# Kernel tuning notes

Hardware: AMD Instinct MI355X
Metric: run time of the kernel (lower is better)

Reference implementation:

```python
import jax, jax.numpy as jnp
import numpy as np

D_MODEL = 1024
N_HEADS = 16
HEAD_DIM = D_MODEL // N_HEADS
EPS = 1e-5


def _rope_tables(T, dim, dtype):
    inv_freq = 1.0 / (10000.0 ** (np.arange(0, dim, 2, dtype=np.float32) / dim))
    t = np.arange(T, dtype=np.float32)
    freqs = np.einsum('i,j->ij', t, inv_freq)            # [T, dim/2]
    emb = np.concatenate([freqs, freqs], axis=-1)        # [T, dim]
    return jnp.asarray(np.cos(emb), dtype), jnp.asarray(np.sin(emb), dtype)


def _rotate(x, cos, sin):
    # x: [B, T, H, hd]; cos/sin: [T, hd] broadcast over B, H
    c = cos[None, :, None, :]
    s = sin[None, :, None, :]
    x1, x2 = jnp.split(x, 2, axis=-1)
    return x * c + jnp.concatenate([-x2, x1], axis=-1) * s


def setup_inputs() -> dict:
    key = jax.random.key(0)
    k1, k2, k3 = jax.random.split(key, 3)
    B, T = 2, 2048
    x = jax.random.normal(k1, (B, T, D_MODEL), jnp.float32)
    norm_w = jnp.ones((D_MODEL,), jnp.float32)
    w_qkv = jax.random.normal(k2, (D_MODEL, 3 * D_MODEL), jnp.float32) * (D_MODEL ** -0.5)
    w_out = jax.random.normal(k3, (D_MODEL, D_MODEL), jnp.float32) * (D_MODEL ** -0.5)
    return {"x": x, "norm_w": norm_w, "w_qkv": w_qkv, "w_out": w_out}


def reference(x, norm_w, w_qkv, w_out):
    B, T, D = x.shape
    residual = x
    # RMSNorm
    h = x * jax.lax.rsqrt(jnp.mean(x * x, axis=-1, keepdims=True) + EPS) * norm_w
    # QKV projection
    qkv = (h @ w_qkv).reshape(B, T, 3, N_HEADS, HEAD_DIM)
    q, k, v = qkv[:, :, 0], qkv[:, :, 1], qkv[:, :, 2]   # [B, T, H, hd]
    # RoPE
    cos, sin = _rope_tables(T, HEAD_DIM, x.dtype)
    q = _rotate(q, cos, sin)
    k = _rotate(k, cos, sin)
    # Non-causal scaled dot-product attention
    scale = HEAD_DIM ** -0.5
    scores = jnp.einsum('bqhd,bkhd->bhqk', q, k) * scale
    attn = jax.nn.softmax(scores, axis=-1)
    out = jnp.einsum('bhqk,bkhd->bqhd', attn, v).reshape(B, T, D)
    return residual + out @ w_out
```

## Files before the change

### kernel.cpp

```cpp
#include <hip/hip_runtime.h>
#include <hip/hip_bf16.h>

typedef float f32x4 __attribute__((ext_vector_type(4)));
typedef __bf16 bf16x8 __attribute__((ext_vector_type(8)));
typedef __bf16 bf16x4 __attribute__((ext_vector_type(4)));

#define D_MODEL 1024
#define T_SEQ   2048
#define NH      16
#define HD      64

__device__ __forceinline__ void gload16(const void* g, void* l) {
    __builtin_amdgcn_global_load_lds(
        (const __attribute__((address_space(1))) unsigned int*)g,
        (__attribute__((address_space(3))) unsigned int*)l, 16, 0, 0);
}

__global__ __launch_bounds__(256) void k_rope_table(float2* __restrict__ tab) {
    int idx = blockIdx.x * 256 + threadIdx.x;
    int t = idx >> 5, i = idx & 31;
    float inv = __builtin_amdgcn_exp2f(-(float)i * 0.41524101186f);
    float ang = (float)t * inv;
    tab[idx] = make_float2(cosf(ang), sinf(ang));
}

__global__ __launch_bounds__(256) void k_rmsnorm(const float* __restrict__ x,
                                                 const float* __restrict__ w,
                                                 __bf16* __restrict__ h) {
    int row = blockIdx.x;
    int tid = threadIdx.x;
    const float4 v = ((const float4*)(x + (size_t)row * D_MODEL))[tid];
    float ss = v.x * v.x + v.y * v.y + v.z * v.z + v.w * v.w;
#pragma unroll
    for (int off = 32; off > 0; off >>= 1) ss += __shfl_down(ss, off, 64);
    __shared__ float red[4];
    if ((tid & 63) == 0) red[tid >> 6] = ss;
    __syncthreads();
    float total = red[0] + red[1] + red[2] + red[3];
    float rms = rsqrtf(total * (1.f / 1024.f) + 1e-5f);
    const float4 wv = ((const float4*)w)[tid];
    bf16x4 o;
    o[0] = (__bf16)(v.x * rms * wv.x);
    o[1] = (__bf16)(v.y * rms * wv.y);
    o[2] = (__bf16)(v.z * rms * wv.z);
    o[3] = (__bf16)(v.w * rms * wv.w);
    ((bf16x4*)(h + (size_t)row * D_MODEL))[tid] = o;
}

__global__ __launch_bounds__(256) void k_transpose_cast(const float* __restrict__ src,
                                                        __bf16* __restrict__ dst,
                                                        int R, int C) {
    __shared__ float tile[32][33];
    int tx = threadIdx.x & 31, ty = threadIdx.x >> 5;
    int c0 = blockIdx.x * 32, r0 = blockIdx.y * 32;
#pragma unroll
    for (int dy = 0; dy < 32; dy += 8)
        tile[ty + dy][tx] = src[(size_t)(r0 + ty + dy) * C + c0 + tx];
    __syncthreads();
#pragma unroll
    for (int dy = 0; dy < 32; dy += 8)
        dst[(size_t)(c0 + ty + dy) * R + r0 + tx] = (__bf16)tile[tx][ty + dy];
}

template <int EPI>
__global__ __launch_bounds__(256) void k_gemm(const __bf16* __restrict__ A,
                                              const __bf16* __restrict__ Bt, int K,
                                              const float2* __restrict__ tab,
                                              __bf16* __restrict__ Qr,
                                              __bf16* __restrict__ Kr,
                                              __bf16* __restrict__ Vt,
                                              const float* __restrict__ resid,
                                              float* __restrict__ outf) {
    __shared__ __bf16 ldsA[128 * 64];
    __shared__ __bf16 ldsB[128 * 64];
    const int tid  = threadIdx.x;
    const int lane = tid & 63;
    const int wave = tid >> 6;
    const int tile_m = blockIdx.y * 128;
    const int tile_n = blockIdx.x * 128;
    const int wm = (wave >> 1) * 64;
    const int wn = (wave & 1) * 64;
    f32x4 acc[4][4] = {};

    const int srow8 = lane >> 3;
    const int sslot = lane & 7;

    for (int k0 = 0; k0 < K; k0 += 64) {
#pragma unroll
        for (int i = 0; i < 4; i++) {
            int rbase = i * 32 + wave * 8;
            int row = rbase + srow8;
            int scol = (sslot ^ (row & 7)) * 8;
            gload16(A  + (size_t)(tile_m + row) * K + k0 + scol,
                    (char*)ldsA + rbase * 128);
            gload16(Bt + (size_t)(tile_n + row) * K + k0 + scol,
                    (char*)ldsB + rbase * 128);
        }
        __syncthreads();
#pragma unroll
        for (int kc = 0; kc < 2; kc++) {
            bf16x8 af[4], bfr[4];
            int s = kc * 4 + (lane >> 4);
#pragma unroll
            for (int mi = 0; mi < 4; mi++) {
                int row = wm + mi * 16 + (lane & 15);
                af[mi] = *(const bf16x8*)((char*)ldsA + row * 128 + ((s ^ (row & 7)) << 4));
            }
#pragma unroll
            for (int nf = 0; nf < 4; nf++) {
                int row = wn + nf * 16 + (lane & 15);
                bfr[nf] = *(const bf16x8*)((char*)ldsB + row * 128 + ((s ^ (row & 7)) << 4));
            }
#pragma unroll
            for (int mi = 0; mi < 4; mi++)
#pragma unroll
                for (int nf = 0; nf < 4; nf++)
                    acc[mi][nf] = __builtin_amdgcn_mfma_f32_16x16x32_bf16(
                        af[mi], bfr[nf], acc[mi][nf], 0, 0, 0);
        }
        __syncthreads();
    }

    if (EPI == 0) {
        const int nb  = tile_n + wn;
        const int sec = nb >> 10;
        const int hh  = (nb & 1023) >> 6;
        if (sec < 2) {
            __bf16* dstbase = (sec == 0) ? Qr : Kr;
            const float sc = (sec == 0) ? 0.180336880111f : 1.0f;
#pragma unroll
            for (int mi = 0; mi < 4; mi++) {
#pragma unroll
                for (int r = 0; r < 4; r++) {
                    int m = tile_m + wm + mi * 16 + (lane >> 4) * 4 + r;
                    int bb = m >> 11, t = m & 2047;
                    float2 cs0 = tab[t * 32 + (lane & 15)];
                    float2 cs1 = tab[t * 32 + 16 + (lane & 15)];
                    float x0 = acc[mi][0][r], x1 = acc[mi][1][r];
                    float x2 = acc[mi][2][r], x3 = acc[mi][3][r];
                    __bf16* dst = dstbase + ((size_t)(bb * NH + hh) * T_SEQ + t) * HD + (lane & 15);
                    dst[0]  = (__bf16)((x0 * cs0.x - x2 * cs0.y) * sc);
                    dst[16] = (__bf16)((x1 * cs1.x - x3 * cs1.y) * sc);
                    dst[32] = (__bf16)((x2 * cs0.x + x0 * cs0.y) * sc);
                    dst[48] = (__bf16)((x3 * cs1.x + x1 * cs1.y) * sc);
                }
            }
        } else {
#pragma unroll
            for (int mi = 0; mi < 4; mi++) {
                int m0 = tile_m + wm + mi * 16 + (lane >> 4) * 4;
                int bb = m0 >> 11, t0 = m0 & 2047;
#pragma unroll
                for (int nf = 0; nf < 4; nf++) {
                    int d = nf * 16 + (lane & 15);
                    bf16x4 pv;
                    pv[0] = (__bf16)acc[mi][nf][0];
                    pv[1] = (__bf16)acc[mi][nf][1];
                    pv[2] = (__bf16)acc[mi][nf][2];
                    pv[3] = (__bf16)acc[mi][nf][3];
                    *(bf16x4*)(Vt + ((size_t)(bb * NH + hh) * HD + d) * T_SEQ + t0) = pv;
                }
            }
        }
    } else {
#pragma unroll
        for (int mi = 0; mi < 4; mi++)
#pragma unroll
            for (int r = 0; r < 4; r++) {
                int m = tile_m + wm + mi * 16 + (lane >> 4) * 4 + r;
#pragma unroll
                for (int nf = 0; nf < 4; nf++) {
                    int n = tile_n + wn + nf * 16 + (lane & 15);
                    size_t idx = (size_t)m * D_MODEL + n;
                    outf[idx] = resid[idx] + acc[mi][nf][r];
                }
            }
    }
}

__global__ __launch_bounds__(256, 4) void k_attn(const __bf16* __restrict__ Qr,
                                                 const __bf16* __restrict__ Kr,
                                                 const __bf16* __restrict__ Vt,
                                                 __bf16* __restrict__ aout) {
    __shared__ __bf16 ldsK[2][64 * 64];
    __shared__ __bf16 ldsV[2][64 * 64];
    __shared__ __bf16 plds_all[4][16 * 64];
    const int lane = threadIdx.x & 63;
    const int wave = threadIdx.x >> 6;
    const int g  = lane >> 4;
    const int lr = lane & 15;

    const int lin = blockIdx.x;
    const int xcd = lin & 7;
    const int idx = lin >> 3;
    const int bh  = xcd * 4 + (idx >> 5);
    const int qb  = idx & 31;
    const int q0  = qb * 64 + wave * 16;

    const __bf16* Q  = Qr + (size_t)bh * T_SEQ * HD;
    const __bf16* Kp = Kr + (size_t)bh * T_SEQ * HD;
    const __bf16* Vp = Vt + (size_t)bh * HD * T_SEQ;
    char* plds = (char*)plds_all[wave];
    char* Kbase = (char*)&ldsK[0][0];
    char* Vbase = (char*)&ldsV[0][0];

    int kofs[2][4], vofs[2][4], pwr[4], prd[2];
#pragma unroll
    for (int kc = 0; kc < 2; kc++)
#pragma unroll
        for (int i = 0; i < 4; i++) {
            int row = i * 16 + lr;
            int sw = (kc * 64 + g * 16) ^ ((row & 7) << 4);
            kofs[kc][i] = row * 128 + sw;
            vofs[kc][i] = row * 128 + sw;
        }
#pragma unroll
    for (int ki = 0; ki < 4; ki++)
        pwr[ki] = lr * 128 + ((ki * 32 + g * 8) ^ ((lr & 7) << 4));
#pragma unroll
    for (int kc = 0; kc < 2; kc++)
        prd[kc] = lr * 128 + ((kc * 64 + g * 16) ^ ((lr & 7) << 4));

    const int srow8 = lane >> 3;
    const int sslot = lane & 7;
    const int scol = (sslot ^ srow8) * 8;
    const int c0 = wave * 2, c1 = wave * 2 + 1;
    const int r0 = c0 * 8 + srow8, r1 = c1 * 8 + srow8;
    const __bf16* kg0 = Kp + (size_t)r0 * HD + scol;
    const __bf16* kg1 = Kp + (size_t)r1 * HD + scol;
    const __bf16* vg0 = Vp + (size_t)r0 * T_SEQ + scol;
    const __bf16* vg1 = Vp + (size_t)r1 * T_SEQ + scol;
    char* Kl0 = Kbase + c0 * 1024;
    char* Kl1 = Kbase + c1 * 1024;
    char* Vl0 = Vbase + c0 * 1024;
    char* Vl1 = Vbase + c1 * 1024;

    bf16x8 qf[2];
#pragma unroll
    for (int kc = 0; kc < 2; kc++)
        qf[kc] = *(const bf16x8*)(Q + (size_t)(q0 + lr) * HD + kc * 32 + g * 8);

    f32x4 o[4] = {};
    float mrun = -1e30f;
    float lrun = 0.f;

    gload16(kg0, Kl0); gload16(kg1, Kl1);
    gload16(vg0, Vl0); gload16(vg1, Vl1);
    kg0 += 64 * HD; kg1 += 64 * HD; vg0 += 64; vg1 += 64;
    __syncthreads();

    for (int tile = 0; tile < 32; tile++) {
        const int bufoff = (tile & 1) << 13;
        if (tile < 31) {
            const int nb = bufoff ^ 8192;
            gload16(kg0, Kl0 + nb); gload16(kg1, Kl1 + nb);
            gload16(vg0, Vl0 + nb); gload16(vg1, Vl1 + nb);
            kg0 += 64 * HD; kg1 += 64 * HD; vg0 += 64; vg1 += 64;
        }

        f32x4 s[4] = {};
        __builtin_amdgcn_s_setprio(1);
#pragma unroll
        for (int kc = 0; kc < 2; kc++) {
            bf16x8 kf[4];
#pragma unroll
            for (int ki = 0; ki < 4; ki++)
                kf[ki] = *(const bf16x8*)(Kbase + bufoff + kofs[kc][ki]);
#pragma unroll
            for (int ki = 0; ki < 4; ki++)
                s[ki] = __builtin_amdgcn_mfma_f32_16x16x32_bf16(
                    kf[ki], qf[kc], s[ki], 0, 0, 0);
        }
        __builtin_amdgcn_s_setprio(0);

        float t0 = fmaxf(fmaxf(s[0][0], s[0][1]), fmaxf(s[0][2], s[0][3]));
        float t1 = fmaxf(fmaxf(s[1][0], s[1][1]), fmaxf(s[1][2], s[1][3]));
        float t2 = fmaxf(fmaxf(s[2][0], s[2][1]), fmaxf(s[2][2], s[2][3]));
        float t3 = fmaxf(fmaxf(s[3][0], s[3][1]), fmaxf(s[3][2], s[3][3]));
        float tv = fmaxf(fmaxf(t0, t1), fmaxf(t2, t3));
        tv = fmaxf(tv, __shfl_xor(tv, 16, 64));
        tv = fmaxf(tv, __shfl_xor(tv, 32, 64));
        if (!__all(tv - mrun <= 8.f)) {
            float mnew = fmaxf(mrun, tv);
            float fac = __builtin_amdgcn_exp2f(mrun - mnew);
            mrun = mnew;
            float facT[4];
#pragma unroll
            for (int r = 0; r < 4; r++)
                facT[r] = __shfl(fac, g * 4 + r, 64);
#pragma unroll
            for (int nf = 0; nf < 4; nf++)
#pragma unroll
                for (int r = 0; r < 4; r++)
                    o[nf][r] *= facT[r];
            lrun *= fac;
        }
        float ts = 0.f;
#pragma unroll
        for (int ki = 0; ki < 4; ki++) {
            float p0 = __builtin_amdgcn_exp2f(s[ki][0] - mrun);
            float p1 = __builtin_amdgcn_exp2f(s[ki][1] - mrun);
            float p2 = __builtin_amdgcn_exp2f(s[ki][2] - mrun);
            float p3 = __builtin_amdgcn_exp2f(s[ki][3] - mrun);
            ts += (p0 + p1) + (p2 + p3);
            bf16x4 pk;
            pk[0] = (__bf16)p0; pk[1] = (__bf16)p1;
            pk[2] = (__bf16)p2; pk[3] = (__bf16)p3;
            *(bf16x4*)(plds + pwr[ki]) = pk;
        }
        bf16x8 vf0[4];
#pragma unroll
        for (int nf = 0; nf < 4; nf++)
            vf0[nf] = *(const bf16x8*)(Vbase + bufoff + vofs[0][nf]);
        ts += __shfl_xor(ts, 16, 64);
        ts += __shfl_xor(ts, 32, 64);
        lrun += ts;

        __builtin_amdgcn_s_setprio(1);
        bf16x8 pf0 = *(const bf16x8*)(plds + prd[0]);
        bf16x8 vf1[4];
#pragma unroll
        for (int nf = 0; nf < 4; nf++)
            vf1[nf] = *(const bf16x8*)(Vbase + bufoff + vofs[1][nf]);
#pragma unroll
        for (int nf = 0; nf < 4; nf++)
            o[nf] = __builtin_amdgcn_mfma_f32_16x16x32_bf16(pf0, vf0[nf], o[nf], 0, 0, 0);
        bf16x8 pf1 = *(const bf16x8*)(plds + prd[1]);
#pragma unroll
        for (int nf = 0; nf < 4; nf++)
            o[nf] = __builtin_amdgcn_mfma_f32_16x16x32_bf16(pf1, vf1[nf], o[nf], 0, 0, 0);
        __builtin_amdgcn_s_setprio(0);
        __syncthreads();
    }

    const int bb = bh >> 4, hh = bh & 15;
    float invT[4];
#pragma unroll
    for (int r = 0; r < 4; r++)
        invT[r] = 1.f / __shfl(lrun, g * 4 + r, 64);
#pragma unroll
    for (int r = 0; r < 4; r++) {
        int t = q0 + g * 4 + r;
#pragma unroll
        for (int nf = 0; nf < 4; nf++) {
            int d = nf * 16 + lr;
            aout[((size_t)(bb * T_SEQ + t)) * D_MODEL + hh * HD + d] =
                (__bf16)(o[nf][r] * invT[r]);
        }
    }
}

extern "C" void kernel_launch(void* const* d_in, const int* in_sizes, int n_in,
                              void* d_out, int out_size, void* d_ws, size_t ws_size,
                              hipStream_t stream) {
    const float* x      = (const float*)d_in[0];
    const float* norm_w = (const float*)d_in[1];
    const float* w_qkv  = (const float*)d_in[2];
    const float* w_out  = (const float*)d_in[3];
    float* out = (float*)d_out;
    char* ws = (char*)d_ws;

    __bf16* hbuf  = (__bf16*)(ws);
    __bf16* wqkvT = (__bf16*)(ws + ((size_t)8  << 20));
    __bf16* woutT = (__bf16*)(ws + ((size_t)14 << 20));
    float2* tab   = (float2*)(ws + ((size_t)16 << 20));
    __bf16* Qr    = (__bf16*)(ws + ((size_t)17 << 20));
    __bf16* Kr    = (__bf16*)(ws + ((size_t)25 << 20));
    __bf16* Vt    = (__bf16*)(ws + ((size_t)33 << 20));

    k_rope_table<<<dim3(256), dim3(256), 0, stream>>>(tab);
    k_rmsnorm<<<dim3(4096), dim3(256), 0, stream>>>(x, norm_w, hbuf);
    k_transpose_cast<<<dim3(96, 32), dim3(256), 0, stream>>>(w_qkv, wqkvT, 1024, 3072);
    k_transpose_cast<<<dim3(32, 32), dim3(256), 0, stream>>>(w_out, woutT, 1024, 1024);
    k_gemm<0><<<dim3(24, 32), dim3(256), 0, stream>>>(hbuf, wqkvT, 1024, tab,
                                                      Qr, Kr, Vt, nullptr, nullptr);
    k_attn<<<dim3(1024), dim3(256), 0, stream>>>(Qr, Kr, Vt, hbuf);
    k_gemm<1><<<dim3(8, 32), dim3(256), 0, stream>>>(hbuf, woutT, 1024, nullptr,
                                                     nullptr, nullptr, nullptr, x, out);
}
```

Baseline: 216.2 us.

## Process two query tiles per wave in attention to reuse K/V fragments

Each wave now handles 32 query rows instead of 16, so each block covers 128 queries and the grid halves to 512 blocks. K and V fragments read from LDS are reused across two MFMA query groups, which halves K/V global traffic and LDS reads per query. The cost is higher register pressure (launch bounds lowered from 4 to 3 blocks), a larger P staging buffer, and fewer blocks to fill the 256 CUs.

```diff
diff --git a/kernel.cpp b/kernel.cpp
--- a/kernel.cpp
+++ b/kernel.cpp
@@ -178,13 +178,13 @@
     }
 }
 
-__global__ __launch_bounds__(256, 4) void k_attn(const __bf16* __restrict__ Qr,
+__global__ __launch_bounds__(256, 3) void k_attn(const __bf16* __restrict__ Qr,
                                                  const __bf16* __restrict__ Kr,
                                                  const __bf16* __restrict__ Vt,
                                                  __bf16* __restrict__ aout) {
     __shared__ __bf16 ldsK[2][64 * 64];
     __shared__ __bf16 ldsV[2][64 * 64];
-    __shared__ __bf16 plds_all[4][16 * 64];
+    __shared__ __bf16 plds_all[4][32 * 64];
     const int lane = threadIdx.x & 63;
     const int wave = threadIdx.x >> 6;
     const int g  = lane >> 4;
@@ -193,9 +193,9 @@
     const int lin = blockIdx.x;
     const int xcd = lin & 7;
     const int idx = lin >> 3;
-    const int bh  = xcd * 4 + (idx >> 5);
-    const int qb  = idx & 31;
-    const int q0  = qb * 64 + wave * 16;
+    const int bh  = xcd * 4 + (idx >> 4);
+    const int qb  = idx & 15;
+    const int q0  = qb * 128 + wave * 32;
 
     const __bf16* Q  = Qr + (size_t)bh * T_SEQ * HD;
     const __bf16* Kp = Kr + (size_t)bh * T_SEQ * HD;
@@ -204,15 +204,13 @@
     char* Kbase = (char*)&ldsK[0][0];
     char* Vbase = (char*)&ldsV[0][0];
 
-    int kofs[2][4], vofs[2][4], pwr[4], prd[2];
+    int kofs[2][4], pwr[4], prd[2];
 #pragma unroll
     for (int kc = 0; kc < 2; kc++)
 #pragma unroll
         for (int i = 0; i < 4; i++) {
             int row = i * 16 + lr;
-            int sw = (kc * 64 + g * 16) ^ ((row & 7) << 4);
-            kofs[kc][i] = row * 128 + sw;
-            vofs[kc][i] = row * 128 + sw;
+            kofs[kc][i] = row * 128 + ((kc * 64 + g * 16) ^ ((row & 7) << 4));
         }
 #pragma unroll
     for (int ki = 0; ki < 4; ki++)
@@ -235,14 +233,17 @@
     char* Vl0 = Vbase + c0 * 1024;
     char* Vl1 = Vbase + c1 * 1024;
 
-    bf16x8 qf[2];
-#pragma unroll
-    for (int kc = 0; kc < 2; kc++)
-        qf[kc] = *(const bf16x8*)(Q + (size_t)(q0 + lr) * HD + kc * 32 + g * 8);
-
-    f32x4 o[4] = {};
-    float mrun = -1e30f;
-    float lrun = 0.f;
+    bf16x8 qf[2][2];
+#pragma unroll
+    for (int qi = 0; qi < 2; qi++)
+#pragma unroll
+        for (int kc = 0; kc < 2; kc++)
+            qf[qi][kc] = *(const bf16x8*)(Q + (size_t)(q0 + qi * 16 + lr) * HD +
+                                          kc * 32 + g * 8);
+
+    f32x4 o[2][4] = {};
+    float mrun[2] = {-1e30f, -1e30f};
+    float lrun[2] = {0.f, 0.f};
 
     gload16(kg0, Kl0); gload16(kg1, Kl1);
     gload16(vg0, Vl0); gload16(vg1, Vl1);
@@ -258,7 +259,7 @@
             kg0 += 64 * HD; kg1 += 64 * HD; vg0 += 64; vg1 += 64;
         }
 
-        f32x4 s[4] = {};
+        f32x4 s[2][4];
         __builtin_amdgcn_s_setprio(1);
 #pragma unroll
         for (int kc = 0; kc < 2; kc++) {
@@ -267,85 +268,101 @@
             for (int ki = 0; ki < 4; ki++)
                 kf[ki] = *(const bf16x8*)(Kbase + bufoff + kofs[kc][ki]);
 #pragma unroll
-            for (int ki = 0; ki < 4; ki++)
-                s[ki] = __builtin_amdgcn_mfma_f32_16x16x32_bf16(
-                    kf[ki], qf[kc], s[ki], 0, 0, 0);
+            for (int qi = 0; qi < 2; qi++)
+#pragma unroll
+                for (int ki = 0; ki < 4; ki++)
+                    s[qi][ki] = (kc == 0)
+                        ? __builtin_amdgcn_mfma_f32_16x16x32_bf16(
+                              kf[ki], qf[qi][0], f32x4{0.f, 0.f, 0.f, 0.f}, 0, 0, 0)
+                        : __builtin_amdgcn_mfma_f32_16x16x32_bf16(
+                              kf[ki], qf[qi][1], s[qi][ki], 0, 0, 0);
         }
         __builtin_amdgcn_s_setprio(0);
 
-        float t0 = fmaxf(fmaxf(s[0][0], s[0][1]), fmaxf(s[0][2], s[0][3]));
-        float t1 = fmaxf(fmaxf(s[1][0], s[1][1]), fmaxf(s[1][2], s[1][3]));
-        float t2 = fmaxf(fmaxf(s[2][0], s[2][1]), fmaxf(s[2][2], s[2][3]));
-        float t3 = fmaxf(fmaxf(s[3][0], s[3][1]), fmaxf(s[3][2], s[3][3]));
-        float tv = fmaxf(fmaxf(t0, t1), fmaxf(t2, t3));
-        tv = fmaxf(tv, __shfl_xor(tv, 16, 64));
-        tv = fmaxf(tv, __shfl_xor(tv, 32, 64));
-        if (!__all(tv - mrun <= 8.f)) {
-            float mnew = fmaxf(mrun, tv);
-            float fac = __builtin_amdgcn_exp2f(mrun - mnew);
-            mrun = mnew;
-            float facT[4];
-#pragma unroll
-            for (int r = 0; r < 4; r++)
-                facT[r] = __shfl(fac, g * 4 + r, 64);
+        float ts2[2];
+#pragma unroll
+        for (int qi = 0; qi < 2; qi++) {
+            float t0 = fmaxf(fmaxf(s[qi][0][0], s[qi][0][1]), fmaxf(s[qi][0][2], s[qi][0][3]));
+            float t1 = fmaxf(fmaxf(s[qi][1][0], s[qi][1][1]), fmaxf(s[qi][1][2], s[qi][1][3]));
+            float t2 = fmaxf(fmaxf(s[qi][2][0], s[qi][2][1]), fmaxf(s[qi][2][2], s[qi][2][3]));
+            float t3 = fmaxf(fmaxf(s[qi][3][0], s[qi][3][1]), fmaxf(s[qi][3][2], s[qi][3][3]));
+            float tv = fmaxf(fmaxf(t0, t1), fmaxf(t2, t3));
+            tv = fmaxf(tv, __shfl_xor(tv, 16, 64));
+            tv = fmaxf(tv, __shfl_xor(tv, 32, 64));
+            if (!__all(tv - mrun[qi] <= 8.f)) {
+                float mnew = fmaxf(mrun[qi], tv);
+                float fac = __builtin_amdgcn_exp2f(mrun[qi] - mnew);
+                mrun[qi] = mnew;
+                float facT[4];
+#pragma unroll
+                for (int r = 0; r < 4; r++)
+                    facT[r] = __shfl(fac, g * 4 + r, 64);
+#pragma unroll
+                for (int nf = 0; nf < 4; nf++)
+#pragma unroll
+                    for (int r = 0; r < 4; r++)
+                        o[qi][nf][r] *= facT[r];
+                lrun[qi] *= fac;
+            }
+            float ts = 0.f;
+#pragma unroll
+            for (int ki = 0; ki < 4; ki++) {
+                float p0 = __builtin_amdgcn_exp2f(s[qi][ki][0] - mrun[qi]);
+                float p1 = __builtin_amdgcn_exp2f(s[qi][ki][1] - mrun[qi]);
+                float p2 = __builtin_amdgcn_exp2f(s[qi][ki][2] - mrun[qi]);
+                float p3 = __builtin_amdgcn_exp2f(s[qi][ki][3] - mrun[qi]);
+                ts += (p0 + p1) + (p2 + p3);
+                bf16x4 pk;
+                pk[0] = (__bf16)p0; pk[1] = (__bf16)p1;
+                pk[2] = (__bf16)p2; pk[3] = (__bf16)p3;
+                *(bf16x4*)(plds + qi * 2048 + pwr[ki]) = pk;
+            }
+            ts2[qi] = ts;
+        }
+#pragma unroll
+        for (int qi = 0; qi < 2; qi++) {
+            float ts = ts2[qi];
+            ts += __shfl_xor(ts, 16, 64);
+            ts += __shfl_xor(ts, 32, 64);
+            lrun[qi] += ts;
+        }
+
+        __builtin_amdgcn_s_setprio(1);
+#pragma unroll
+        for (int kc = 0; kc < 2; kc++) {
+            bf16x8 vf[4];
 #pragma unroll
             for (int nf = 0; nf < 4; nf++)
-#pragma unroll
-                for (int r = 0; r < 4; r++)
-                    o[nf][r] *= facT[r];
-            lrun *= fac;
-        }
-        float ts = 0.f;
-#pragma unroll
-        for (int ki = 0; ki < 4; ki++) {
-            float p0 = __builtin_amdgcn_exp2f(s[ki][0] - mrun);
-            float p1 = __builtin_amdgcn_exp2f(s[ki][1] - mrun);
-            float p2 = __builtin_amdgcn_exp2f(s[ki][2] - mrun);
-            float p3 = __builtin_amdgcn_exp2f(s[ki][3] - mrun);
-            ts += (p0 + p1) + (p2 + p3);
-            bf16x4 pk;
-            pk[0] = (__bf16)p0; pk[1] = (__bf16)p1;
-            pk[2] = (__bf16)p2; pk[3] = (__bf16)p3;
-            *(bf16x4*)(plds + pwr[ki]) = pk;
-        }
-        bf16x8 vf0[4];
-#pragma unroll
-        for (int nf = 0; nf < 4; nf++)
-            vf0[nf] = *(const bf16x8*)(Vbase + bufoff + vofs[0][nf]);
-        ts += __shfl_xor(ts, 16, 64);
-        ts += __shfl_xor(ts, 32, 64);
-        lrun += ts;
-
-        __builtin_amdgcn_s_setprio(1);
-        bf16x8 pf0 = *(const bf16x8*)(plds + prd[0]);
-        bf16x8 vf1[4];
-#pragma unroll
-        for (int nf = 0; nf < 4; nf++)
-            vf1[nf] = *(const bf16x8*)(Vbase + bufoff + vofs[1][nf]);
-#pragma unroll
-        for (int nf = 0; nf < 4; nf++)
-            o[nf] = __builtin_amdgcn_mfma_f32_16x16x32_bf16(pf0, vf0[nf], o[nf], 0, 0, 0);
-        bf16x8 pf1 = *(const bf16x8*)(plds + prd[1]);
-#pragma unroll
-        for (int nf = 0; nf < 4; nf++)
-            o[nf] = __builtin_amdgcn_mfma_f32_16x16x32_bf16(pf1, vf1[nf], o[nf], 0, 0, 0);
+                vf[nf] = *(const bf16x8*)(Vbase + bufoff + kofs[kc][nf]);
+            bf16x8 pf0 = *(const bf16x8*)(plds + prd[kc]);
+            bf16x8 pf1 = *(const bf16x8*)(plds + 2048 + prd[kc]);
+#pragma unroll
+            for (int nf = 0; nf < 4; nf++)
+                o[0][nf] = __builtin_amdgcn_mfma_f32_16x16x32_bf16(pf0, vf[nf], o[0][nf], 0, 0, 0);
+#pragma unroll
+            for (int nf = 0; nf < 4; nf++)
+                o[1][nf] = __builtin_amdgcn_mfma_f32_16x16x32_bf16(pf1, vf[nf], o[1][nf], 0, 0, 0);
+        }
         __builtin_amdgcn_s_setprio(0);
         __syncthreads();
     }
 
     const int bb = bh >> 4, hh = bh & 15;
-    float invT[4];
-#pragma unroll
-    for (int r = 0; r < 4; r++)
-        invT[r] = 1.f / __shfl(lrun, g * 4 + r, 64);
-#pragma unroll
-    for (int r = 0; r < 4; r++) {
-        int t = q0 + g * 4 + r;
-#pragma unroll
-        for (int nf = 0; nf < 4; nf++) {
-            int d = nf * 16 + lr;
-            aout[((size_t)(bb * T_SEQ + t)) * D_MODEL + hh * HD + d] =
-                (__bf16)(o[nf][r] * invT[r]);
+#pragma unroll
+    for (int qi = 0; qi < 2; qi++) {
+        float invT[4];
+#pragma unroll
+        for (int r = 0; r < 4; r++)
+            invT[r] = 1.f / __shfl(lrun[qi], g * 4 + r, 64);
+#pragma unroll
+        for (int r = 0; r < 4; r++) {
+            int t = q0 + qi * 16 + g * 4 + r;
+#pragma unroll
+            for (int nf = 0; nf < 4; nf++) {
+                int d = nf * 16 + lr;
+                aout[((size_t)(bb * T_SEQ + t)) * D_MODEL + hh * HD + d] =
+                    (__bf16)(o[qi][nf][r] * invT[r]);
+            }
         }
     }
 }
@@ -374,7 +391,7 @@
     k_transpose_cast<<<dim3(32, 32), dim3(256), 0, stream>>>(w_out, woutT, 1024, 1024);
     k_gemm<0><<<dim3(24, 32), dim3(256), 0, stream>>>(hbuf, wqkvT, 1024, tab,
                                                       Qr, Kr, Vt, nullptr, nullptr);
-    k_attn<<<dim3(1024), dim3(256), 0, stream>>>(Qr, Kr, Vt, hbuf);
+    k_attn<<<dim3(512), dim3(256), 0, stream>>>(Qr, Kr, Vt, hbuf);
     k_gemm<1><<<dim3(8, 32), dim3(256), 0, stream>>>(hbuf, woutT, 1024, nullptr,
                                                      nullptr, nullptr, nullptr, x, out);
 }
```

Result: no change. 215.5 us (-0.4%).
